# Kernel tuning notes

Hardware: AMD Instinct MI355X
Metric: run time of the kernel (lower is better)

The kernel has to match this reference:

```python
import jax, jax.numpy as jnp
import numpy as np

NU, NT, E, H, NL, NVOC, OUT, HID2 = 100000, 400000, 400000, 128, 3, 10000, 2, 64
EPS = 1e-5


def setup_inputs() -> dict:
    key = jax.random.key(0)
    ks = jax.random.split(key, 20)
    s = 1.0 / np.sqrt(H).astype(np.float32)
    inp = {
        "x_user": jax.random.randint(ks[0], (NU,), 0, NVOC),
        "x_txn": jax.random.randint(ks[1], (NT,), 0, NVOC),
        "ei0_src": jax.random.randint(ks[2], (E,), 0, NU),
        "ei0_dst": jax.random.randint(ks[3], (E,), 0, NT),
        "ei1_src": jax.random.randint(ks[4], (E,), 0, NT),
        "ei1_dst": jax.random.randint(ks[5], (E,), 0, NU),
        "emb_user": jax.random.normal(ks[6], (NVOC, H), jnp.float32),
        "emb_txn": jax.random.normal(ks[7], (NVOC, H), jnp.float32),
        "Wl": jax.random.normal(ks[8], (NL, 2, H, H), jnp.float32) * s,
        "bl": jax.random.normal(ks[9], (NL, 2, H), jnp.float32) * 0.01,
        "Wr": jax.random.normal(ks[10], (NL, 2, H, H), jnp.float32) * s,
        "bn_gamma": jax.random.uniform(ks[11], (NL, 2, H), jnp.float32, 0.5, 1.5),
        "bn_beta": jax.random.normal(ks[12], (NL, 2, H), jnp.float32) * 0.01,
        "bn_mean": jax.random.normal(ks[13], (NL, 2, H), jnp.float32) * 0.01,
        "bn_var": jax.random.uniform(ks[14], (NL, 2, H), jnp.float32, 0.5, 1.5),
        "W1": jax.random.normal(ks[15], (H, HID2), jnp.float32) * s,
        "b1": jax.random.normal(ks[16], (HID2,), jnp.float32) * 0.01,
        "W2": jax.random.normal(ks[17], (HID2, OUT), jnp.float32) * (1.0 / np.sqrt(HID2).astype(np.float32)),
        "b2": jax.random.normal(ks[18], (OUT,), jnp.float32) * 0.01,
    }
    return inp


def _seg_mean(src_feat, src_idx, dst_idx, num_dst):
    # gather per-edge src features, mean-reduce per dst node (SAGEConv aggr='mean')
    msg = src_feat[src_idx]                                        # [E, H]
    tot = jax.ops.segment_sum(msg, dst_idx, num_segments=num_dst)  # [Ndst, H]
    cnt = jax.ops.segment_sum(jnp.ones((dst_idx.shape[0], 1), src_feat.dtype),
                              dst_idx, num_segments=num_dst)
    return tot / jnp.maximum(cnt, 1.0)


def _bn_relu(x, g, b, m, v):
    return jax.nn.relu((x - m) * jax.lax.rsqrt(v + EPS) * g + b)


def reference(x_user, x_txn, ei0_src, ei0_dst, ei1_src, ei1_dst,
              emb_user, emb_txn, Wl, bl, Wr,
              bn_gamma, bn_beta, bn_mean, bn_var, W1, b1, W2, b2):
    h_u = emb_user[x_user]   # [NU, H]
    h_t = emb_txn[x_txn]     # [NT, H]
    for i in range(NL):
        # edge type 0: user -> transaction; edge type 1: transaction -> user
        agg_t = _seg_mean(h_u, ei0_src, ei0_dst, h_t.shape[0])
        agg_u = _seg_mean(h_t, ei1_src, ei1_dst, h_u.shape[0])
        new_t = agg_t @ Wl[i, 0] + bl[i, 0] + h_t @ Wr[i, 0]
        new_u = agg_u @ Wl[i, 1] + bl[i, 1] + h_u @ Wr[i, 1]
        h_u = _bn_relu(new_u, bn_gamma[i, 0], bn_beta[i, 0], bn_mean[i, 0], bn_var[i, 0])
        h_t = _bn_relu(new_t, bn_gamma[i, 1], bn_beta[i, 1], bn_mean[i, 1], bn_var[i, 1])
    h = jnp.concatenate([h_u, h_t], axis=0)            # [NU+NT, H]
    out = jax.nn.relu(h @ W1 + b1) @ W2 + b2           # [NU+NT, OUT]
    return out
```

## Files before the change

### kernel.cpp

```cpp
#include <hip/hip_runtime.h>


#define NUv   100000
#define NTv   400000
#define Ev    400000
#define Hv    128
#define NLv   3
#define HID2v 64
#define EPSv  1e-5f

typedef _Float16 h16;
typedef __attribute__((ext_vector_type(8))) _Float16 f16x8;
typedef __attribute__((ext_vector_type(4))) float    f32x4;

#define WS_NEED (280u * 1024u * 1024u)
__device__ __attribute__((aligned(256))) static unsigned char g_ws[WS_NEED];

__device__ __forceinline__ int imin(int a, int b) { return a < b ? a : b; }
__device__ __forceinline__ int swz(int n, int kbyte) {
  return n * 256 + (kbyte ^ ((n & 7) << 4));
}
__device__ __forceinline__ int swzB(int n, int kbyte) {
  return n * 512 + (kbyte ^ ((n & 7) << 4));
}

__global__ __launch_bounds__(256) void k_count(const int* __restrict__ d0,
                                               const int* __restrict__ d1,
                                               int* __restrict__ c0,
                                               int* __restrict__ c1, int e) {
  int t = blockIdx.x * 256 + threadIdx.x;
  if (t < e) {
    atomicAdd(c0 + d0[t], 1);
    atomicAdd(c1 + d1[t], 1);
  }
}

__global__ __launch_bounds__(256) void k_blocksum(const int* __restrict__ cnt,
                                                  int* __restrict__ bs, int n) {
  __shared__ int red[256];
  int base = blockIdx.x * 2048 + threadIdx.x * 8;
  int s = 0;
#pragma unroll
  for (int j = 0; j < 8; j++) {
    int p = base + j;
    if (p < n) s += cnt[p];
  }
  red[threadIdx.x] = s;
  __syncthreads();
  for (int st = 128; st > 0; st >>= 1) {
    if (threadIdx.x < st) red[threadIdx.x] += red[threadIdx.x + st];
    __syncthreads();
  }
  if (threadIdx.x == 0) bs[blockIdx.x] = red[0];
}

__global__ __launch_bounds__(256) void k_scansmall(int* __restrict__ bs, int g) {
  __shared__ int lds[256];
  int t = threadIdx.x;
  int v = (t < g) ? bs[t] : 0;
  lds[t] = v;
  __syncthreads();
  for (int st = 1; st < 256; st <<= 1) {
    int x = (t >= st) ? lds[t - st] : 0;
    __syncthreads();
    lds[t] += x;
    __syncthreads();
  }
  if (t < g) bs[t] = lds[t] - v;
}

__global__ __launch_bounds__(256) void k_scanfinal(const int* __restrict__ cnt,
                                                   const int* __restrict__ bs,
                                                   int* __restrict__ off,
                                                   int* __restrict__ cur, int n) {
  __shared__ int lds[256];
  int t = threadIdx.x;
  int base = blockIdx.x * 2048 + t * 8;
  int v[8], pre[8];
  int tsum = 0;
#pragma unroll
  for (int j = 0; j < 8; j++) {
    int p = base + j;
    v[j] = (p < n) ? cnt[p] : 0;
    pre[j] = tsum;
    tsum += v[j];
  }
  lds[t] = tsum;
  __syncthreads();
  for (int st = 1; st < 256; st <<= 1) {
    int x = (t >= st) ? lds[t - st] : 0;
    __syncthreads();
    lds[t] += x;
    __syncthreads();
  }
  int texcl = lds[t] - tsum;
  int boff = bs[blockIdx.x];
#pragma unroll
  for (int j = 0; j < 8; j++) {
    int p = base + j;
    if (p < n) {
      int o = boff + texcl + pre[j];
      off[p] = o;
      cur[p] = o;
      if (p == n - 1) off[n] = o + v[j];
    }
  }
}

__global__ __launch_bounds__(256) void k_fill(const int* __restrict__ s0,
                                              const int* __restrict__ d0,
                                              const int* __restrict__ s1,
                                              const int* __restrict__ d1,
                                              int* __restrict__ cur0,
                                              int* __restrict__ cur1,
                                              int* __restrict__ ss0,
                                              int* __restrict__ ss1, int e) {
  int t = blockIdx.x * 256 + threadIdx.x;
  if (t < e) {
    int p = atomicAdd(cur0 + d0[t], 1);
    ss0[p] = s0[t];
    int q = atomicAdd(cur1 + d1[t], 1);
    ss1[q] = s1[t];
  }
}

__global__ __launch_bounds__(256) void k_wt(const float* __restrict__ Wl,
                                            const float* __restrict__ Wr,
                                            const float* __restrict__ W1,
                                            h16* __restrict__ WlT,
                                            h16* __restrict__ WrT,
                                            h16* __restrict__ W1T) {
  int t = blockIdx.x * 256 + threadIdx.x;
  const int NW = NLv * 2 * Hv * Hv;
  if (t < NW) {
    int mat = t / (Hv * Hv);
    int n = (t / Hv) % Hv;
    int k = t % Hv;
    WlT[t] = (h16)Wl[(size_t)mat * Hv * Hv + (size_t)k * Hv + n];
    WrT[t] = (h16)Wr[(size_t)mat * Hv * Hv + (size_t)k * Hv + n];
  } else if (t < NW + HID2v * Hv) {
    int u = t - NW;
    int n = u / Hv;
    int k = u % Hv;
    W1T[u] = (h16)W1[(size_t)k * HID2v + n];
  }
}

__global__ __launch_bounds__(256) void k_bn(const float* __restrict__ g,
                                            const float* __restrict__ b,
                                            const float* __restrict__ m,
                                            const float* __restrict__ v,
                                            float* __restrict__ sc,
                                            float* __restrict__ sh) {
  int t = blockIdx.x * 256 + threadIdx.x;
  if (t < NLv * 2 * Hv) {
    float inv = rsqrtf(v[t] + EPSv);
    float s = g[t] * inv;
    sc[t] = s;
    sh[t] = b[t] - m[t] * s;
  }
}

__global__ __launch_bounds__(256) void k_embed(const int* __restrict__ xu,
                                               const int* __restrict__ xt,
                                               const float* __restrict__ eu,
                                               const float* __restrict__ et,
                                               h16* __restrict__ hu,
                                               h16* __restrict__ ht) {
  int t = blockIdx.x * 256 + threadIdx.x;
  int row = t >> 4;
  int c = (t & 15) * 8;
  if (row >= NUv + NTv) return;
  const float* src;
  h16* dst;
  if (row < NUv) {
    src = eu + (size_t)xu[row] * Hv;
    dst = hu + (size_t)row * Hv;
  } else {
    int r2 = row - NUv;
    src = et + (size_t)xt[r2] * Hv;
    dst = ht + (size_t)r2 * Hv;
  }
  float4 v0 = *(const float4*)(src + c);
  float4 v1 = *(const float4*)(src + c + 4);
  f16x8 o;
  o[0] = (h16)v0.x; o[1] = (h16)v0.y; o[2] = (h16)v0.z; o[3] = (h16)v0.w;
  o[4] = (h16)v1.x; o[5] = (h16)v1.y; o[6] = (h16)v1.z; o[7] = (h16)v1.w;
  *(f16x8*)(dst + c) = o;
}

__global__ __launch_bounds__(512, 4) void k_fused(const h16* __restrict__ SRC,
                                                  const h16* __restrict__ DENSE,
                                                  const int* __restrict__ off,
                                                  const int* __restrict__ ss,
                                                  const h16* __restrict__ BTl,
                                                  const h16* __restrict__ BTr,
                                                  const float* __restrict__ bl,
                                                  const float* __restrict__ sc,
                                                  const float* __restrict__ sh,
                                                  h16* __restrict__ C, int M) {
  __shared__ __align__(16) unsigned char sB[128 * 512];
  __shared__ __align__(16) unsigned char sA[64 * 256];

  int t = threadIdx.x;
  int l = t & 63;
  int lm = l & 15, lk = l >> 4;
  int w = t >> 6;
  int rg = w >> 1, cg = w & 1;

  {
    int n = t >> 2;
    int kb = (t & 3) * 64;
    const h16* sr = BTr + t * 32;
    f16x8 r0 = *(const f16x8*)(sr + 0);
    f16x8 r1 = *(const f16x8*)(sr + 8);
    f16x8 r2 = *(const f16x8*)(sr + 16);
    f16x8 r3 = *(const f16x8*)(sr + 24);
    const h16* sl = BTl + t * 32;
    f16x8 l0 = *(const f16x8*)(sl + 0);
    f16x8 l1 = *(const f16x8*)(sl + 8);
    f16x8 l2 = *(const f16x8*)(sl + 16);
    f16x8 l3 = *(const f16x8*)(sl + 24);
    *(f16x8*)(sB + swzB(n, kb + 0)) = r0;
    *(f16x8*)(sB + swzB(n, kb + 16)) = r1;
    *(f16x8*)(sB + swzB(n, kb + 32)) = r2;
    *(f16x8*)(sB + swzB(n, kb + 48)) = r3;
    *(f16x8*)(sB + swzB(n, 256 + kb + 0)) = l0;
    *(f16x8*)(sB + swzB(n, 256 + kb + 16)) = l1;
    *(f16x8*)(sB + swzB(n, 256 + kb + 32)) = l2;
    *(f16x8*)(sB + swzB(n, 256 + kb + 48)) = l3;
  }
  __syncthreads();

  int nTiles = (M + 63) / 64;
  for (int tile = blockIdx.x; tile < nTiles; tile += gridDim.x) {
    int base = tile * 64;

    int ar = imin(base + rg * 16 + lm, M - 1);
    const h16* arow = DENSE + (size_t)ar * Hv;
    f16x8 ad0 = *(const f16x8*)(arow + 0 * 32 + lk * 8);
    f16x8 ad1 = *(const f16x8*)(arow + 1 * 32 + lk * 8);
    f16x8 ad2 = *(const f16x8*)(arow + 2 * 32 + lk * 8);
    f16x8 ad3 = *(const f16x8*)(arow + 3 * 32 + lk * 8);

    {
      int r = t >> 3;
      int cs = (t & 7) * 16;
      float facc[16];
#pragma unroll
      for (int j = 0; j < 16; j++) facc[j] = 0.f;
      int row = base + r;
      if (row < M) {
        int e0 = off[row], e1 = off[row + 1];
        for (int e = e0; e < e1; e += 2) {
          int i0 = ss[e];
          bool v1 = (e + 1) < e1;
          int i1 = v1 ? ss[e + 1] : i0;
          const f16x8* p0 = (const f16x8*)(SRC + (size_t)i0 * Hv + cs);
          const f16x8* p1 = (const f16x8*)(SRC + (size_t)i1 * Hv + cs);
          f16x8 x0 = p0[0], x1 = p0[1];
          f16x8 y0 = p1[0], y1 = p1[1];
          float m1 = v1 ? 1.f : 0.f;
#pragma unroll
          for (int j = 0; j < 8; j++) {
            facc[j] += (float)x0[j];
            facc[8 + j] += (float)x1[j];
            facc[j] = fmaf((float)y0[j], m1, facc[j]);
            facc[8 + j] = fmaf((float)y1[j], m1, facc[8 + j]);
          }
        }
        int deg = e1 - e0;
        float inv = 1.f / (float)(deg > 1 ? deg : 1);
#pragma unroll
        for (int j = 0; j < 16; j++) facc[j] *= inv;
      }
#pragma unroll
      for (int q = 0; q < 2; q++) {
        f16x8 ov;
#pragma unroll
        for (int j = 0; j < 8; j++) ov[j] = (h16)facc[q * 8 + j];
        *(f16x8*)(sA + swz(r, cs * 2 + q * 16)) = ov;
      }
    }
    __syncthreads();

    f32x4 acc[4];
#pragma unroll
    for (int j = 0; j < 4; j++) acc[j] = (f32x4){0.f, 0.f, 0.f, 0.f};
    {
      f16x8 ads[4] = {ad0, ad1, ad2, ad3};
#pragma unroll
      for (int s = 0; s < 4; s++) {
#pragma unroll
        for (int j = 0; j < 4; j++) {
          int n = (cg * 4 + j) * 16 + lm;
          f16x8 b = *(const f16x8*)(sB + swzB(n, s * 64 + lk * 16));
          acc[j] = __builtin_amdgcn_mfma_f32_16x16x32_f16(ads[s], b, acc[j], 0, 0, 0);
        }
      }
#pragma unroll
      for (int s = 0; s < 4; s++) {
        f16x8 a = *(const f16x8*)(sA + swz(rg * 16 + lm, s * 64 + lk * 16));
#pragma unroll
        for (int j = 0; j < 4; j++) {
          int n = (cg * 4 + j) * 16 + lm;
          f16x8 b = *(const f16x8*)(sB + swzB(n, 256 + s * 64 + lk * 16));
          acc[j] = __builtin_amdgcn_mfma_f32_16x16x32_f16(a, b, acc[j], 0, 0, 0);
        }
      }
    }

#pragma unroll
    for (int j = 0; j < 4; j++) {
      int col = (cg * 4 + j) * 16 + lm;
      float blv = bl[col], scv = sc[col], shv = sh[col];
#pragma unroll
      for (int r_ = 0; r_ < 4; r_++) {
        int row = base + rg * 16 + lk * 4 + r_;
        if (row < M) {
          float x = fmaf(acc[j][r_] + blv, scv, shv);
          C[(size_t)row * Hv + col] = (h16)fmaxf(x, 0.f);
        }
      }
    }
    __syncthreads();
  }
}

__global__ __launch_bounds__(512, 4) void k_mlp(const h16* __restrict__ HU,
                                                const h16* __restrict__ HT,
                                                const h16* __restrict__ W1T,
                                                const float* __restrict__ b1,
                                                const float* __restrict__ W2,
                                                const float* __restrict__ b2,
                                                float* __restrict__ out, int Mtot) {
  __shared__ float y[128][65];
  __shared__ __align__(16) unsigned char sW[64 * 256];
  int t = threadIdx.x;
  int w = t >> 6, l = t & 63;
  int lm = l & 15, lk = l >> 4;

  {
    const h16* src = W1T + t * 16;
    f16x8 w0 = *(const f16x8*)(src + 0);
    f16x8 w1 = *(const f16x8*)(src + 8);
    int n = (t * 16) >> 7;
    int kb = ((t * 16) & 127) * 2;
    *(f16x8*)(sW + swz(n, kb + 0)) = w0;
    *(f16x8*)(sW + swz(n, kb + 16)) = w1;
  }

  int rowBase = blockIdx.x * 128 + w * 16;
  int ar = imin(rowBase + lm, Mtot - 1);
  const h16* arow =
      (ar < NUv) ? (HU + (size_t)ar * Hv) : (HT + (size_t)(ar - NUv) * Hv);
  f16x8 a0 = *(const f16x8*)(arow + 0 * 32 + lk * 8);
  f16x8 a1 = *(const f16x8*)(arow + 1 * 32 + lk * 8);
  f16x8 a2 = *(const f16x8*)(arow + 2 * 32 + lk * 8);
  f16x8 a3 = *(const f16x8*)(arow + 3 * 32 + lk * 8);
  __syncthreads();

  f32x4 acc[4];
#pragma unroll
  for (int nf = 0; nf < 4; nf++) acc[nf] = (f32x4){0.f, 0.f, 0.f, 0.f};
  {
    f16x8 as[4] = {a0, a1, a2, a3};
#pragma unroll
    for (int s = 0; s < 4; s++) {
#pragma unroll
      for (int nf = 0; nf < 4; nf++) {
        f16x8 b = *(const f16x8*)(sW + swz(nf * 16 + lm, s * 64 + lk * 16));
        acc[nf] = __builtin_amdgcn_mfma_f32_16x16x32_f16(as[s], b, acc[nf], 0, 0, 0);
      }
    }
  }
#pragma unroll
  for (int nf = 0; nf < 4; nf++) {
    int col = nf * 16 + lm;
    float b1v = b1[col];
#pragma unroll
    for (int r = 0; r < 4; r++) {
      int rloc = w * 16 + lk * 4 + r;
      y[rloc][col] = fmaxf(acc[nf][r] + b1v, 0.f);
    }
  }
  __syncthreads();
  if (t < 256) {
    int rloc = t >> 1, o = t & 1;
    int row = blockIdx.x * 128 + rloc;
    if (row < Mtot) {
      float sum = b2[o];
#pragma unroll
      for (int k = 0; k < HID2v; k++) sum += y[rloc][k] * W2[k * 2 + o];
      out[(size_t)row * 2 + o] = sum;
    }
  }
}

extern "C" void kernel_launch(void* const* d_in, const int* in_sizes, int n_in,
                              void* d_out, int out_size, void* d_ws, size_t ws_size,
                              hipStream_t stream) {
  (void)in_sizes; (void)n_in; (void)out_size;

  const int* x_user  = (const int*)d_in[0];
  const int* x_txn   = (const int*)d_in[1];
  const int* ei0_src = (const int*)d_in[2];
  const int* ei0_dst = (const int*)d_in[3];
  const int* ei1_src = (const int*)d_in[4];
  const int* ei1_dst = (const int*)d_in[5];
  const float* emb_user = (const float*)d_in[6];
  const float* emb_txn  = (const float*)d_in[7];
  const float* Wl = (const float*)d_in[8];
  const float* bl = (const float*)d_in[9];
  const float* Wr = (const float*)d_in[10];
  const float* bn_g = (const float*)d_in[11];
  const float* bn_b = (const float*)d_in[12];
  const float* bn_m = (const float*)d_in[13];
  const float* bn_v = (const float*)d_in[14];
  const float* W1 = (const float*)d_in[15];
  const float* b1 = (const float*)d_in[16];
  const float* W2 = (const float*)d_in[17];
  const float* b2 = (const float*)d_in[18];
  float* out = (float*)d_out;

  char* wsb;
  if (ws_size >= (size_t)WS_NEED) {
    wsb = (char*)d_ws;
  } else {
    void* sym = nullptr;
    hipGetSymbolAddress(&sym, HIP_SYMBOL(g_ws));
    wsb = (char*)sym;
  }
  size_t o = 0;
  auto alloc = [&](size_t bytes) -> void* {
    o = (o + 255) & ~(size_t)255;
    void* p = wsb + o;
    o += bytes;
    return p;
  };
  h16* hu   = (h16*)alloc((size_t)NUv * Hv * 2);
  h16* ht0  = (h16*)alloc((size_t)NTv * Hv * 2);
  h16* ht1  = (h16*)alloc((size_t)NTv * Hv * 2);
  h16* WlT  = (h16*)alloc((size_t)NLv * 2 * Hv * Hv * 2);
  h16* WrT  = (h16*)alloc((size_t)NLv * 2 * Hv * Hv * 2);
  h16* W1T  = (h16*)alloc((size_t)HID2v * Hv * 2);
  float* bnsc = (float*)alloc((size_t)NLv * 2 * Hv * 4);
  float* bnsh = (float*)alloc((size_t)NLv * 2 * Hv * 4);
  int* off0 = (int*)alloc((size_t)(NTv + 1) * 4);
  int* off1 = (int*)alloc((size_t)(NUv + 1) * 4);
  int* cur0 = (int*)alloc((size_t)NTv * 4);
  int* cur1 = (int*)alloc((size_t)NUv * 4);
  int* ss0  = (int*)alloc((size_t)Ev * 4);
  int* ss1  = (int*)alloc((size_t)Ev * 4);
  int* bs0  = (int*)alloc(256 * 4);
  int* bs1  = (int*)alloc(256 * 4);

  const int G_E    = (Ev + 255) / 256;
  const int G_BS0  = (NTv + 2047) / 2048;
  const int G_BS1  = (NUv + 2047) / 2048;
  const int G_EMB  = ((NUv + NTv) * 16 + 255) / 256;
  const int G_WT   = (NLv * 2 * Hv * Hv + HID2v * Hv + 255) / 256;
  const int G_F    = 512;
  const int G_MLP  = (NUv + NTv + 127) / 128;

  hipMemsetAsync(cur0, 0, (size_t)NTv * 4, stream);
  hipMemsetAsync(cur1, 0, (size_t)NUv * 4, stream);
  k_count<<<G_E, 256, 0, stream>>>(ei0_dst, ei1_dst, cur0, cur1, Ev);
  k_blocksum<<<G_BS0, 256, 0, stream>>>(cur0, bs0, NTv);
  k_blocksum<<<G_BS1, 256, 0, stream>>>(cur1, bs1, NUv);
  k_scansmall<<<1, 256, 0, stream>>>(bs0, G_BS0);
  k_scansmall<<<1, 256, 0, stream>>>(bs1, G_BS1);
  k_scanfinal<<<G_BS0, 256, 0, stream>>>(cur0, bs0, off0, cur0, NTv);
  k_scanfinal<<<G_BS1, 256, 0, stream>>>(cur1, bs1, off1, cur1, NUv);
  k_fill<<<G_E, 256, 0, stream>>>(ei0_src, ei0_dst, ei1_src, ei1_dst,
                                  cur0, cur1, ss0, ss1, Ev);

  k_wt<<<G_WT, 256, 0, stream>>>(Wl, Wr, W1, WlT, WrT, W1T);
  k_bn<<<3, 256, 0, stream>>>(bn_g, bn_b, bn_m, bn_v, bnsc, bnsh);

  k_embed<<<G_EMB, 256, 0, stream>>>(x_user, x_txn, emb_user, emb_txn, hu, ht0);

  h16* ht_cur = ht0; h16* ht_nxt = ht1;
  for (int i = 0; i < NLv; i++) {
    const h16* WlT0 = WlT + (size_t)(i * 2 + 0) * Hv * Hv;
    const h16* WlT1 = WlT + (size_t)(i * 2 + 1) * Hv * Hv;
    const h16* WrT0 = WrT + (size_t)(i * 2 + 0) * Hv * Hv;
    const h16* WrT1 = WrT + (size_t)(i * 2 + 1) * Hv * Hv;
    const float* bl0 = bl + (size_t)(i * 2 + 0) * Hv;
    const float* bl1 = bl + (size_t)(i * 2 + 1) * Hv;
    const float* sc0 = bnsc + (size_t)(i * 2 + 0) * Hv;
    const float* sh0 = bnsh + (size_t)(i * 2 + 0) * Hv;
    const float* sc1 = bnsc + (size_t)(i * 2 + 1) * Hv;
    const float* sh1 = bnsh + (size_t)(i * 2 + 1) * Hv;

    k_fused<<<G_F, 512, 0, stream>>>(hu, ht_cur, off0, ss0, WlT0, WrT0,
                                     bl0, sc1, sh1, ht_nxt, NTv);
    k_fused<<<G_F, 512, 0, stream>>>(ht_cur, hu, off1, ss1, WlT1, WrT1,
                                     bl1, sc0, sh0, hu, NUv);
    h16* tmp = ht_cur; ht_cur = ht_nxt; ht_nxt = tmp;
  }

  k_mlp<<<G_MLP, 512, 0, stream>>>(hu, ht_cur, W1T, b1, W2, b2, out, NUv + NTv);
}
```

Before: 660.4 us.

## Double-buffer gathered aggregate tile and keep Wr weights in registers

The fused SAGE kernel now gathers the neighbor mean for the next tile into a second shared-memory buffer while computing the MFMA GEMM for the current tile, removing one barrier per tile. The Wr weight fragments are held in registers instead of shared memory, which halves the shared B buffer. The user feature buffer is also double-buffered so the in-place hu update cannot race with the prefetched gathers. This raises register pressure under a 512x4 launch bound and may cause spills or lower occupancy.

```diff
diff --git a/kernel.cpp b/kernel.cpp
--- a/kernel.cpp
+++ b/kernel.cpp
@@ -19,9 +19,6 @@
 __device__ __forceinline__ int imin(int a, int b) { return a < b ? a : b; }
 __device__ __forceinline__ int swz(int n, int kbyte) {
   return n * 256 + (kbyte ^ ((n & 7) << 4));
-}
-__device__ __forceinline__ int swzB(int n, int kbyte) {
-  return n * 512 + (kbyte ^ ((n & 7) << 4));
 }
 
 __global__ __launch_bounds__(256) void k_count(const int* __restrict__ d0,
@@ -199,42 +196,87 @@
                                                   const float* __restrict__ sc,
                                                   const float* __restrict__ sh,
                                                   h16* __restrict__ C, int M) {
-  __shared__ __align__(16) unsigned char sB[128 * 512];
-  __shared__ __align__(16) unsigned char sA[64 * 256];
+  __shared__ __align__(16) unsigned char sB[128 * 256];
+  __shared__ __align__(16) unsigned char sA[2][64 * 256];
 
   int t = threadIdx.x;
-  int l = t & 63;
-  int lm = l & 15, lk = l >> 4;
-  int w = t >> 6;
-  int rg = w >> 1, cg = w & 1;
+  int l = t & 63, lm = l & 15, lk = l >> 4;
+  int w = t >> 6, rg = w >> 1, cg = w & 1;
+  int r = t >> 3, cs = (t & 7) * 16;
+
+  f16x8 bR[16];
+#pragma unroll
+  for (int s = 0; s < 4; s++)
+#pragma unroll
+    for (int j = 0; j < 4; j++)
+      bR[s * 4 + j] = *(const f16x8*)(BTr +
+          (size_t)((cg * 4 + j) * 16 + lm) * Hv + s * 32 + lk * 8);
 
   {
     int n = t >> 2;
     int kb = (t & 3) * 64;
-    const h16* sr = BTr + t * 32;
-    f16x8 r0 = *(const f16x8*)(sr + 0);
-    f16x8 r1 = *(const f16x8*)(sr + 8);
-    f16x8 r2 = *(const f16x8*)(sr + 16);
-    f16x8 r3 = *(const f16x8*)(sr + 24);
     const h16* sl = BTl + t * 32;
     f16x8 l0 = *(const f16x8*)(sl + 0);
     f16x8 l1 = *(const f16x8*)(sl + 8);
     f16x8 l2 = *(const f16x8*)(sl + 16);
     f16x8 l3 = *(const f16x8*)(sl + 24);
-    *(f16x8*)(sB + swzB(n, kb + 0)) = r0;
-    *(f16x8*)(sB + swzB(n, kb + 16)) = r1;
-    *(f16x8*)(sB + swzB(n, kb + 32)) = r2;
-    *(f16x8*)(sB + swzB(n, kb + 48)) = r3;
-    *(f16x8*)(sB + swzB(n, 256 + kb + 0)) = l0;
-    *(f16x8*)(sB + swzB(n, 256 + kb + 16)) = l1;
-    *(f16x8*)(sB + swzB(n, 256 + kb + 32)) = l2;
-    *(f16x8*)(sB + swzB(n, 256 + kb + 48)) = l3;
-  }
+    *(f16x8*)(sB + swz(n, kb + 0)) = l0;
+    *(f16x8*)(sB + swz(n, kb + 16)) = l1;
+    *(f16x8*)(sB + swz(n, kb + 32)) = l2;
+    *(f16x8*)(sB + swz(n, kb + 48)) = l3;
+  }
+
+  int nTiles = (M + 63) / 64;
+
+  auto gather = [&](int gtile, int buf) {
+    unsigned char* sAw = &sA[buf][0];
+    float facc[16];
+#pragma unroll
+    for (int j = 0; j < 16; j++) facc[j] = 0.f;
+    int row = gtile * 64 + r;
+    if (row < M) {
+      int e0 = off[row], e1 = off[row + 1];
+      for (int e = e0; e < e1; e += 2) {
+        int i0 = ss[e];
+        bool v1 = (e + 1) < e1;
+        int i1 = v1 ? ss[e + 1] : i0;
+        const f16x8* p0 = (const f16x8*)(SRC + (size_t)i0 * Hv + cs);
+        const f16x8* p1 = (const f16x8*)(SRC + (size_t)i1 * Hv + cs);
+        f16x8 x0 = p0[0], x1 = p0[1];
+        f16x8 y0 = p1[0], y1 = p1[1];
+        float m1 = v1 ? 1.f : 0.f;
+#pragma unroll
+        for (int j = 0; j < 8; j++) {
+          facc[j] += (float)x0[j];
+          facc[8 + j] += (float)x1[j];
+          facc[j] = fmaf((float)y0[j], m1, facc[j]);
+          facc[8 + j] = fmaf((float)y1[j], m1, facc[8 + j]);
+        }
+      }
+      int deg = e1 - e0;
+      float inv = 1.f / (float)(deg > 1 ? deg : 1);
+#pragma unroll
+      for (int j = 0; j < 16; j++) facc[j] *= inv;
+    }
+#pragma unroll
+    for (int q = 0; q < 2; q++) {
+      f16x8 ov;
+#pragma unroll
+      for (int j = 0; j < 8; j++) ov[j] = (h16)facc[q * 8 + j];
+      *(f16x8*)(sAw + swz(r, cs * 2 + q * 16)) = ov;
+    }
+  };
+
+  int tile = blockIdx.x;
+  if (tile < nTiles) gather(tile, 0);
   __syncthreads();
 
-  int nTiles = (M + 63) / 64;
-  for (int tile = blockIdx.x; tile < nTiles; tile += gridDim.x) {
+  int bb = 0;
+  for (; tile < nTiles; tile += gridDim.x) {
     int base = tile * 64;
+    int nxt = tile + gridDim.x;
+
+    if (nxt < nTiles) gather(nxt, bb ^ 1);
 
     int ar = imin(base + rg * 16 + lm, M - 1);
     const h16* arow = DENSE + (size_t)ar * Hv;
@@ -243,71 +285,29 @@
     f16x8 ad2 = *(const f16x8*)(arow + 2 * 32 + lk * 8);
     f16x8 ad3 = *(const f16x8*)(arow + 3 * 32 + lk * 8);
 
-    {
-      int r = t >> 3;
-      int cs = (t & 7) * 16;
-      float facc[16];
-#pragma unroll
-      for (int j = 0; j < 16; j++) facc[j] = 0.f;
-      int row = base + r;
-      if (row < M) {
-        int e0 = off[row], e1 = off[row + 1];
-        for (int e = e0; e < e1; e += 2) {
-          int i0 = ss[e];
-          bool v1 = (e + 1) < e1;
-          int i1 = v1 ? ss[e + 1] : i0;
-          const f16x8* p0 = (const f16x8*)(SRC + (size_t)i0 * Hv + cs);
-          const f16x8* p1 = (const f16x8*)(SRC + (size_t)i1 * Hv + cs);
-          f16x8 x0 = p0[0], x1 = p0[1];
-          f16x8 y0 = p1[0], y1 = p1[1];
-          float m1 = v1 ? 1.f : 0.f;
-#pragma unroll
-          for (int j = 0; j < 8; j++) {
-            facc[j] += (float)x0[j];
-            facc[8 + j] += (float)x1[j];
-            facc[j] = fmaf((float)y0[j], m1, facc[j]);
-            facc[8 + j] = fmaf((float)y1[j], m1, facc[8 + j]);
-          }
-        }
-        int deg = e1 - e0;
-        float inv = 1.f / (float)(deg > 1 ? deg : 1);
-#pragma unroll
-        for (int j = 0; j < 16; j++) facc[j] *= inv;
+    f32x4 acc[4];
+#pragma unroll
+    for (int j = 0; j < 4; j++) acc[j] = (f32x4){0.f, 0.f, 0.f, 0.f};
+
+    const unsigned char* sAr = &sA[bb][0];
+#pragma unroll
+    for (int s = 0; s < 4; s++) {
+      f16x8 a = *(const f16x8*)(sAr + swz(rg * 16 + lm, s * 64 + lk * 16));
+#pragma unroll
+      for (int j = 0; j < 4; j++) {
+        int n = (cg * 4 + j) * 16 + lm;
+        f16x8 b = *(const f16x8*)(sB + swz(n, s * 64 + lk * 16));
+        acc[j] = __builtin_amdgcn_mfma_f32_16x16x32_f16(a, b, acc[j], 0, 0, 0);
       }
-#pragma unroll
-      for (int q = 0; q < 2; q++) {
-        f16x8 ov;
-#pragma unroll
-        for (int j = 0; j < 8; j++) ov[j] = (h16)facc[q * 8 + j];
-        *(f16x8*)(sA + swz(r, cs * 2 + q * 16)) = ov;
-      }
-    }
-    __syncthreads();
-
-    f32x4 acc[4];
-#pragma unroll
-    for (int j = 0; j < 4; j++) acc[j] = (f32x4){0.f, 0.f, 0.f, 0.f};
+    }
     {
       f16x8 ads[4] = {ad0, ad1, ad2, ad3};
 #pragma unroll
-      for (int s = 0; s < 4; s++) {
-#pragma unroll
-        for (int j = 0; j < 4; j++) {
-          int n = (cg * 4 + j) * 16 + lm;
-          f16x8 b = *(const f16x8*)(sB + swzB(n, s * 64 + lk * 16));
-          acc[j] = __builtin_amdgcn_mfma_f32_16x16x32_f16(ads[s], b, acc[j], 0, 0, 0);
-        }
-      }
-#pragma unroll
-      for (int s = 0; s < 4; s++) {
-        f16x8 a = *(const f16x8*)(sA + swz(rg * 16 + lm, s * 64 + lk * 16));
-#pragma unroll
-        for (int j = 0; j < 4; j++) {
-          int n = (cg * 4 + j) * 16 + lm;
-          f16x8 b = *(const f16x8*)(sB + swzB(n, 256 + s * 64 + lk * 16));
-          acc[j] = __builtin_amdgcn_mfma_f32_16x16x32_f16(a, b, acc[j], 0, 0, 0);
-        }
-      }
+      for (int s = 0; s < 4; s++)
+#pragma unroll
+        for (int j = 0; j < 4; j++)
+          acc[j] = __builtin_amdgcn_mfma_f32_16x16x32_f16(ads[s], bR[s * 4 + j],
+                                                          acc[j], 0, 0, 0);
     }
 
 #pragma unroll
@@ -324,6 +324,7 @@
       }
     }
     __syncthreads();
+    bb ^= 1;
   }
 }
 
@@ -438,7 +439,8 @@
     o += bytes;
     return p;
   };
-  h16* hu   = (h16*)alloc((size_t)NUv * Hv * 2);
+  h16* hu0  = (h16*)alloc((size_t)NUv * Hv * 2);
+  h16* hu1  = (h16*)alloc((size_t)NUv * Hv * 2);
   h16* ht0  = (h16*)alloc((size_t)NTv * Hv * 2);
   h16* ht1  = (h16*)alloc((size_t)NTv * Hv * 2);
   h16* WlT  = (h16*)alloc((size_t)NLv * 2 * Hv * Hv * 2);
@@ -478,8 +480,9 @@
   k_wt<<<G_WT, 256, 0, stream>>>(Wl, Wr, W1, WlT, WrT, W1T);
   k_bn<<<3, 256, 0, stream>>>(bn_g, bn_b, bn_m, bn_v, bnsc, bnsh);
 
-  k_embed<<<G_EMB, 256, 0, stream>>>(x_user, x_txn, emb_user, emb_txn, hu, ht0);
-
+  k_embed<<<G_EMB, 256, 0, stream>>>(x_user, x_txn, emb_user, emb_txn, hu0, ht0);
+
+  h16* hu_cur = hu0; h16* hu_nxt = hu1;
   h16* ht_cur = ht0; h16* ht_nxt = ht1;
   for (int i = 0; i < NLv; i++) {
     const h16* WlT0 = WlT + (size_t)(i * 2 + 0) * Hv * Hv;
@@ -493,12 +496,15 @@
     const float* sc1 = bnsc + (size_t)(i * 2 + 1) * Hv;
     const float* sh1 = bnsh + (size_t)(i * 2 + 1) * Hv;
 
-    k_fused<<<G_F, 512, 0, stream>>>(hu, ht_cur, off0, ss0, WlT0, WrT0,
+    k_fused<<<G_F, 512, 0, stream>>>(hu_cur, ht_cur, off0, ss0, WlT0, WrT0,
                                      bl0, sc1, sh1, ht_nxt, NTv);
-    k_fused<<<G_F, 512, 0, stream>>>(ht_cur, hu, off1, ss1, WlT1, WrT1,
-                                     bl1, sc0, sh0, hu, NUv);
-    h16* tmp = ht_cur; ht_cur = ht_nxt; ht_nxt = tmp;
-  }
-
-  k_mlp<<<G_MLP, 512, 0, stream>>>(hu, ht_cur, W1T, b1, W2, b2, out, NUv + NTv);
-}
+    k_fused<<<G_F, 512, 0, stream>>>(ht_cur, hu_cur, off1, ss1, WlT1, WrT1,
+                                     bl1, sc0, sh0, hu_nxt, NUv);
+    h16* tmp;
+    tmp = ht_cur; ht_cur = ht_nxt; ht_nxt = tmp;
+    tmp = hu_cur; hu_cur = hu_nxt; hu_nxt = tmp;
+  }
+
+  k_mlp<<<G_MLP, 512, 0, stream>>>(hu_cur, ht_cur, W1T, b1, W2, b2, out,
+                                   NUv + NTv);
+}
```

Result: slower. 730.9 us (+10.7%).

## Merge per-direction launches into combined kernels and double-buffer user features

Applied to the files above, without the earlier changes.

Each GNN layer now runs both message-passing directions in one fused kernel launch over a combined tile space, and weights are reloaded into shared memory only when a block crosses to the other direction. Running both directions concurrently requires a second user-feature buffer, since the user-side output can no longer overwrite its input in place. The paired blocksum, scan and final-scan kernels are likewise merged into single launches, and the weight-transpose and batch-norm kernels are combined. This is meant to remove launch overhead and the tail idle time between the two directions, at the cost of extra workspace and per-tile branching.

```diff
diff --git a/kernel.cpp b/kernel.cpp
--- a/kernel.cpp
+++ b/kernel.cpp
@@ -35,10 +35,19 @@
   }
 }
 
-__global__ __launch_bounds__(256) void k_blocksum(const int* __restrict__ cnt,
-                                                  int* __restrict__ bs, int n) {
+__global__ __launch_bounds__(256) void k_blocksum2(const int* __restrict__ c0,
+                                                   int n0, int g0,
+                                                   const int* __restrict__ c1,
+                                                   int n1,
+                                                   int* __restrict__ bs0,
+                                                   int* __restrict__ bs1) {
   __shared__ int red[256];
-  int base = blockIdx.x * 2048 + threadIdx.x * 8;
+  int second = blockIdx.x >= g0 ? 1 : 0;
+  const int* cnt = second ? c1 : c0;
+  int n = second ? n1 : n0;
+  int* bs = second ? bs1 : bs0;
+  int bid = blockIdx.x - (second ? g0 : 0);
+  int base = bid * 2048 + threadIdx.x * 8;
   int s = 0;
 #pragma unroll
   for (int j = 0; j < 8; j++) {
@@ -51,11 +60,14 @@
     if (threadIdx.x < st) red[threadIdx.x] += red[threadIdx.x + st];
     __syncthreads();
   }
-  if (threadIdx.x == 0) bs[blockIdx.x] = red[0];
-}
-
-__global__ __launch_bounds__(256) void k_scansmall(int* __restrict__ bs, int g) {
+  if (threadIdx.x == 0) bs[bid] = red[0];
+}
+
+__global__ __launch_bounds__(256) void k_scansmall2(int* __restrict__ bs0, int g0,
+                                                    int* __restrict__ bs1, int g1) {
   __shared__ int lds[256];
+  int* bs = blockIdx.x ? bs1 : bs0;
+  int g = blockIdx.x ? g1 : g0;
   int t = threadIdx.x;
   int v = (t < g) ? bs[t] : 0;
   lds[t] = v;
@@ -69,13 +81,26 @@
   if (t < g) bs[t] = lds[t] - v;
 }
 
-__global__ __launch_bounds__(256) void k_scanfinal(const int* __restrict__ cnt,
-                                                   const int* __restrict__ bs,
-                                                   int* __restrict__ off,
-                                                   int* __restrict__ cur, int n) {
+__global__ __launch_bounds__(256) void k_scanfinal2(const int* __restrict__ c0,
+                                                    int n0, int g0,
+                                                    const int* __restrict__ bs0,
+                                                    int* __restrict__ off0,
+                                                    int* __restrict__ cur0,
+                                                    const int* __restrict__ c1,
+                                                    int n1,
+                                                    const int* __restrict__ bs1,
+                                                    int* __restrict__ off1,
+                                                    int* __restrict__ cur1) {
   __shared__ int lds[256];
+  int second = blockIdx.x >= g0 ? 1 : 0;
+  const int* cnt = second ? c1 : c0;
+  const int* bs = second ? bs1 : bs0;
+  int* off = second ? off1 : off0;
+  int* cur = second ? cur1 : cur0;
+  int n = second ? n1 : n0;
+  int bid = blockIdx.x - (second ? g0 : 0);
   int t = threadIdx.x;
-  int base = blockIdx.x * 2048 + t * 8;
+  int base = bid * 2048 + t * 8;
   int v[8], pre[8];
   int tsum = 0;
 #pragma unroll
@@ -94,7 +119,7 @@
     __syncthreads();
   }
   int texcl = lds[t] - tsum;
-  int boff = bs[blockIdx.x];
+  int boff = bs[bid];
 #pragma unroll
   for (int j = 0; j < 8; j++) {
     int p = base + j;
@@ -124,40 +149,38 @@
   }
 }
 
-__global__ __launch_bounds__(256) void k_wt(const float* __restrict__ Wl,
-                                            const float* __restrict__ Wr,
-                                            const float* __restrict__ W1,
-                                            h16* __restrict__ WlT,
-                                            h16* __restrict__ WrT,
-                                            h16* __restrict__ W1T) {
+__global__ __launch_bounds__(256) void k_wtbn(const float* __restrict__ Wl,
+                                              const float* __restrict__ Wr,
+                                              const float* __restrict__ W1,
+                                              const float* __restrict__ g,
+                                              const float* __restrict__ b,
+                                              const float* __restrict__ m,
+                                              const float* __restrict__ v,
+                                              h16* __restrict__ WlT,
+                                              h16* __restrict__ WrT,
+                                              h16* __restrict__ W1T,
+                                              float* __restrict__ sc,
+                                              float* __restrict__ sh) {
   int t = blockIdx.x * 256 + threadIdx.x;
   const int NW = NLv * 2 * Hv * Hv;
+  const int NW1 = NW + HID2v * Hv;
   if (t < NW) {
     int mat = t / (Hv * Hv);
     int n = (t / Hv) % Hv;
     int k = t % Hv;
     WlT[t] = (h16)Wl[(size_t)mat * Hv * Hv + (size_t)k * Hv + n];
     WrT[t] = (h16)Wr[(size_t)mat * Hv * Hv + (size_t)k * Hv + n];
-  } else if (t < NW + HID2v * Hv) {
+  } else if (t < NW1) {
     int u = t - NW;
     int n = u / Hv;
     int k = u % Hv;
     W1T[u] = (h16)W1[(size_t)k * HID2v + n];
-  }
-}
-
-__global__ __launch_bounds__(256) void k_bn(const float* __restrict__ g,
-                                            const float* __restrict__ b,
-                                            const float* __restrict__ m,
-                                            const float* __restrict__ v,
-                                            float* __restrict__ sc,
-                                            float* __restrict__ sh) {
-  int t = blockIdx.x * 256 + threadIdx.x;
-  if (t < NLv * 2 * Hv) {
-    float inv = rsqrtf(v[t] + EPSv);
-    float s = g[t] * inv;
-    sc[t] = s;
-    sh[t] = b[t] - m[t] * s;
+  } else if (t < NW1 + NLv * 2 * Hv) {
+    int u = t - NW1;
+    float inv = rsqrtf(v[u] + EPSv);
+    float s = g[u] * inv;
+    sc[u] = s;
+    sh[u] = b[u] - m[u] * s;
   }
 }
 
@@ -189,52 +212,68 @@
   *(f16x8*)(dst + c) = o;
 }
 
-__global__ __launch_bounds__(512, 4) void k_fused(const h16* __restrict__ SRC,
-                                                  const h16* __restrict__ DENSE,
-                                                  const int* __restrict__ off,
-                                                  const int* __restrict__ ss,
-                                                  const h16* __restrict__ BTl,
-                                                  const h16* __restrict__ BTr,
-                                                  const float* __restrict__ bl,
-                                                  const float* __restrict__ sc,
-                                                  const float* __restrict__ sh,
-                                                  h16* __restrict__ C, int M) {
+__global__ __launch_bounds__(512, 4) void k_fused2(
+    const h16* __restrict__ SRC0, const h16* __restrict__ DEN0,
+    const int* __restrict__ offA, const int* __restrict__ ssA,
+    const h16* __restrict__ BTl0, const h16* __restrict__ BTr0,
+    const float* __restrict__ blp0, const float* __restrict__ scp0,
+    const float* __restrict__ shp0, h16* __restrict__ C0, int M0,
+    const h16* __restrict__ SRC1, const h16* __restrict__ DEN1,
+    const int* __restrict__ offB, const int* __restrict__ ssB,
+    const h16* __restrict__ BTl1, const h16* __restrict__ BTr1,
+    const float* __restrict__ blp1, const float* __restrict__ scp1,
+    const float* __restrict__ shp1, h16* __restrict__ C1, int M1) {
   __shared__ __align__(16) unsigned char sB[128 * 512];
   __shared__ __align__(16) unsigned char sA[64 * 256];
 
   int t = threadIdx.x;
-  int l = t & 63;
-  int lm = l & 15, lk = l >> 4;
-  int w = t >> 6;
-  int rg = w >> 1, cg = w & 1;
-
-  {
-    int n = t >> 2;
-    int kb = (t & 3) * 64;
-    const h16* sr = BTr + t * 32;
-    f16x8 r0 = *(const f16x8*)(sr + 0);
-    f16x8 r1 = *(const f16x8*)(sr + 8);
-    f16x8 r2 = *(const f16x8*)(sr + 16);
-    f16x8 r3 = *(const f16x8*)(sr + 24);
-    const h16* sl = BTl + t * 32;
-    f16x8 l0 = *(const f16x8*)(sl + 0);
-    f16x8 l1 = *(const f16x8*)(sl + 8);
-    f16x8 l2 = *(const f16x8*)(sl + 16);
-    f16x8 l3 = *(const f16x8*)(sl + 24);
-    *(f16x8*)(sB + swzB(n, kb + 0)) = r0;
-    *(f16x8*)(sB + swzB(n, kb + 16)) = r1;
-    *(f16x8*)(sB + swzB(n, kb + 32)) = r2;
-    *(f16x8*)(sB + swzB(n, kb + 48)) = r3;
-    *(f16x8*)(sB + swzB(n, 256 + kb + 0)) = l0;
-    *(f16x8*)(sB + swzB(n, 256 + kb + 16)) = l1;
-    *(f16x8*)(sB + swzB(n, 256 + kb + 32)) = l2;
-    *(f16x8*)(sB + swzB(n, 256 + kb + 48)) = l3;
-  }
-  __syncthreads();
-
-  int nTiles = (M + 63) / 64;
-  for (int tile = blockIdx.x; tile < nTiles; tile += gridDim.x) {
-    int base = tile * 64;
+  int l = t & 63, lm = l & 15, lk = l >> 4;
+  int w = t >> 6, rg = w >> 1, cg = w & 1;
+
+  int nT0 = (M0 + 63) / 64;
+  int nT1 = (M1 + 63) / 64;
+  int nTot = nT0 + nT1;
+  int curDir = -1;
+
+  for (int gidx = blockIdx.x; gidx < nTot; gidx += gridDim.x) {
+    int dir = (gidx < nT0) ? 0 : 1;
+    const h16* SRC = dir ? SRC1 : SRC0;
+    const h16* DENSE = dir ? DEN1 : DEN0;
+    const int* off = dir ? offB : offA;
+    const int* ss = dir ? ssB : ssA;
+    const float* blp = dir ? blp1 : blp0;
+    const float* scp = dir ? scp1 : scp0;
+    const float* shp = dir ? shp1 : shp0;
+    h16* C = dir ? C1 : C0;
+    int M = dir ? M1 : M0;
+    int base = (dir ? gidx - nT0 : gidx) * 64;
+
+    if (dir != curDir) {
+      const h16* BTr = dir ? BTr1 : BTr0;
+      const h16* BTl = dir ? BTl1 : BTl0;
+      int n = t >> 2;
+      int kb = (t & 3) * 64;
+      const h16* sr = BTr + t * 32;
+      f16x8 r0 = *(const f16x8*)(sr + 0);
+      f16x8 r1 = *(const f16x8*)(sr + 8);
+      f16x8 r2 = *(const f16x8*)(sr + 16);
+      f16x8 r3 = *(const f16x8*)(sr + 24);
+      const h16* sl = BTl + t * 32;
+      f16x8 l0 = *(const f16x8*)(sl + 0);
+      f16x8 l1 = *(const f16x8*)(sl + 8);
+      f16x8 l2 = *(const f16x8*)(sl + 16);
+      f16x8 l3 = *(const f16x8*)(sl + 24);
+      *(f16x8*)(sB + swzB(n, kb + 0)) = r0;
+      *(f16x8*)(sB + swzB(n, kb + 16)) = r1;
+      *(f16x8*)(sB + swzB(n, kb + 32)) = r2;
+      *(f16x8*)(sB + swzB(n, kb + 48)) = r3;
+      *(f16x8*)(sB + swzB(n, 256 + kb + 0)) = l0;
+      *(f16x8*)(sB + swzB(n, 256 + kb + 16)) = l1;
+      *(f16x8*)(sB + swzB(n, 256 + kb + 32)) = l2;
+      *(f16x8*)(sB + swzB(n, 256 + kb + 48)) = l3;
+      __syncthreads();
+      curDir = dir;
+    }
 
     int ar = imin(base + rg * 16 + lm, M - 1);
     const h16* arow = DENSE + (size_t)ar * Hv;
@@ -313,7 +352,7 @@
 #pragma unroll
     for (int j = 0; j < 4; j++) {
       int col = (cg * 4 + j) * 16 + lm;
-      float blv = bl[col], scv = sc[col], shv = sh[col];
+      float blv = blp[col], scv = scp[col], shv = shp[col];
 #pragma unroll
       for (int r_ = 0; r_ < 4; r_++) {
         int row = base + rg * 16 + lk * 4 + r_;
@@ -438,7 +477,8 @@
     o += bytes;
     return p;
   };
-  h16* hu   = (h16*)alloc((size_t)NUv * Hv * 2);
+  h16* hu0  = (h16*)alloc((size_t)NUv * Hv * 2);
+  h16* hu1  = (h16*)alloc((size_t)NUv * Hv * 2);
   h16* ht0  = (h16*)alloc((size_t)NTv * Hv * 2);
   h16* ht1  = (h16*)alloc((size_t)NTv * Hv * 2);
   h16* WlT  = (h16*)alloc((size_t)NLv * 2 * Hv * Hv * 2);
@@ -459,27 +499,29 @@
   const int G_BS0  = (NTv + 2047) / 2048;
   const int G_BS1  = (NUv + 2047) / 2048;
   const int G_EMB  = ((NUv + NTv) * 16 + 255) / 256;
-  const int G_WT   = (NLv * 2 * Hv * Hv + HID2v * Hv + 255) / 256;
+  const int N_WTBN = NLv * 2 * Hv * Hv + HID2v * Hv + NLv * 2 * Hv;
+  const int G_WTBN = (N_WTBN + 255) / 256;
   const int G_F    = 512;
   const int G_MLP  = (NUv + NTv + 127) / 128;
 
   hipMemsetAsync(cur0, 0, (size_t)NTv * 4, stream);
   hipMemsetAsync(cur1, 0, (size_t)NUv * 4, stream);
   k_count<<<G_E, 256, 0, stream>>>(ei0_dst, ei1_dst, cur0, cur1, Ev);
-  k_blocksum<<<G_BS0, 256, 0, stream>>>(cur0, bs0, NTv);
-  k_blocksum<<<G_BS1, 256, 0, stream>>>(cur1, bs1, NUv);
-  k_scansmall<<<1, 256, 0, stream>>>(bs0, G_BS0);
-  k_scansmall<<<1, 256, 0, stream>>>(bs1, G_BS1);
-  k_scanfinal<<<G_BS0, 256, 0, stream>>>(cur0, bs0, off0, cur0, NTv);
-  k_scanfinal<<<G_BS1, 256, 0, stream>>>(cur1, bs1, off1, cur1, NUv);
+  k_blocksum2<<<G_BS0 + G_BS1, 256, 0, stream>>>(cur0, NTv, G_BS0, cur1, NUv,
+                                                 bs0, bs1);
+  k_scansmall2<<<2, 256, 0, stream>>>(bs0, G_BS0, bs1, G_BS1);
+  k_scanfinal2<<<G_BS0 + G_BS1, 256, 0, stream>>>(cur0, NTv, G_BS0, bs0, off0,
+                                                  cur0, cur1, NUv, bs1, off1,
+                                                  cur1);
   k_fill<<<G_E, 256, 0, stream>>>(ei0_src, ei0_dst, ei1_src, ei1_dst,
                                   cur0, cur1, ss0, ss1, Ev);
 
-  k_wt<<<G_WT, 256, 0, stream>>>(Wl, Wr, W1, WlT, WrT, W1T);
-  k_bn<<<3, 256, 0, stream>>>(bn_g, bn_b, bn_m, bn_v, bnsc, bnsh);
-
-  k_embed<<<G_EMB, 256, 0, stream>>>(x_user, x_txn, emb_user, emb_txn, hu, ht0);
-
+  k_wtbn<<<G_WTBN, 256, 0, stream>>>(Wl, Wr, W1, bn_g, bn_b, bn_m, bn_v,
+                                     WlT, WrT, W1T, bnsc, bnsh);
+
+  k_embed<<<G_EMB, 256, 0, stream>>>(x_user, x_txn, emb_user, emb_txn, hu0, ht0);
+
+  h16* hu_cur = hu0; h16* hu_nxt = hu1;
   h16* ht_cur = ht0; h16* ht_nxt = ht1;
   for (int i = 0; i < NLv; i++) {
     const h16* WlT0 = WlT + (size_t)(i * 2 + 0) * Hv * Hv;
@@ -493,12 +535,14 @@
     const float* sc1 = bnsc + (size_t)(i * 2 + 1) * Hv;
     const float* sh1 = bnsh + (size_t)(i * 2 + 1) * Hv;
 
-    k_fused<<<G_F, 512, 0, stream>>>(hu, ht_cur, off0, ss0, WlT0, WrT0,
-                                     bl0, sc1, sh1, ht_nxt, NTv);
-    k_fused<<<G_F, 512, 0, stream>>>(ht_cur, hu, off1, ss1, WlT1, WrT1,
-                                     bl1, sc0, sh0, hu, NUv);
-    h16* tmp = ht_cur; ht_cur = ht_nxt; ht_nxt = tmp;
-  }
-
-  k_mlp<<<G_MLP, 512, 0, stream>>>(hu, ht_cur, W1T, b1, W2, b2, out, NUv + NTv);
-}
+    k_fused2<<<G_F, 512, 0, stream>>>(
+        hu_cur, ht_cur, off0, ss0, WlT0, WrT0, bl0, sc1, sh1, ht_nxt, NTv,
+        ht_cur, hu_cur, off1, ss1, WlT1, WrT1, bl1, sc0, sh0, hu_nxt, NUv);
+    h16* tmp;
+    tmp = ht_cur; ht_cur = ht_nxt; ht_nxt = tmp;
+    tmp = hu_cur; hu_cur = hu_nxt; hu_nxt = tmp;
+  }
+
+  k_mlp<<<G_MLP, 512, 0, stream>>>(hu_cur, ht_cur, W1T, b1, W2, b2, out,
+                                   NUv + NTv);
+}
```

Measured after the change: 706.8 us. +7.0%, slower.
